# Kernel optimization log

Measured on AMD Instinct MI355X. Metric: run time of the kernel, lower is better.

## Reference

```python
import jax, jax.numpy as jnp
import numpy as np

E = 2048
H = 16
DH = E // H  # 128
B, T = 2, 2048
EPS = 1e-8


def rmsnorm(x, g):
    rms = jnp.sqrt(jnp.mean(x * x, axis=-1, keepdims=True) + EPS)
    return g * (x / rms)


def setup_inputs() -> dict:
    key = jax.random.key(0)
    ks = jax.random.split(key, 16)
    s_in = 1.0 / np.sqrt(E)
    s_ff = 1.0 / np.sqrt(4 * E)
    return {
        "x": jax.random.normal(ks[0], (B, T, E), dtype=jnp.float32),
        # stacked per-head QKV projections, stored (in, out) so y = x @ W + b
        "wq": jax.random.normal(ks[1], (H, E, DH), dtype=jnp.float32) * s_in,
        "bq": jax.random.normal(ks[2], (H, DH), dtype=jnp.float32) * s_in,
        "wk": jax.random.normal(ks[3], (H, E, DH), dtype=jnp.float32) * s_in,
        "bk": jax.random.normal(ks[4], (H, DH), dtype=jnp.float32) * s_in,
        "wv": jax.random.normal(ks[5], (H, E, DH), dtype=jnp.float32) * s_in,
        "bv": jax.random.normal(ks[6], (H, DH), dtype=jnp.float32) * s_in,
        "wo": jax.random.normal(ks[7], (E, E), dtype=jnp.float32) * s_in,
        "bo": jax.random.normal(ks[8], (E,), dtype=jnp.float32) * s_in,
        "w1": jax.random.normal(ks[9], (E, 4 * E), dtype=jnp.float32) * s_in,
        "b1": jax.random.normal(ks[10], (4 * E,), dtype=jnp.float32) * s_in,
        "w2": jax.random.normal(ks[11], (4 * E, E), dtype=jnp.float32) * s_ff,
        "b2": jax.random.normal(ks[12], (E,), dtype=jnp.float32) * s_ff,
        "g1": jnp.ones((E,), dtype=jnp.float32),
        "g2": jnp.ones((E,), dtype=jnp.float32),
    }


def reference(x, wq, bq, wk, bk, wv, bv, wo, bo, w1, b1, w2, b2, g1, g2):
    b, t, e = x.shape
    # --- attention sublayer ---
    h = rmsnorm(x, g1)
    q = jnp.einsum("bte,hed->bhtd", h, wq) + bq[None, :, None, :]
    k = jnp.einsum("bte,hed->bhtd", h, wk) + bk[None, :, None, :]
    v = jnp.einsum("bte,hed->bhtd", h, wv) + bv[None, :, None, :]
    scores = jnp.einsum("bhtd,bhsd->bhts", q, k) / jnp.sqrt(jnp.float32(DH))
    causal = jnp.tril(jnp.ones((t, t), dtype=bool))
    scores = jnp.where(causal[None, None], scores, -jnp.inf)
    w = jax.nn.softmax(scores, axis=-1)
    o = jnp.einsum("bhts,bhsd->bhtd", w, v)
    o = o.transpose(0, 2, 1, 3).reshape(b, t, e)  # concat heads on last dim
    x = x + o @ wo + bo
    # --- FFN sublayer (exact GELU, dropout is identity at inference) ---
    h = rmsnorm(x, g2)
    x = x + jax.nn.gelu(h @ w1 + b1, approximate=False) @ w2 + b2
    return x
```

## Files before the change

kernel.cpp:

```cpp
#include <hip/hip_runtime.h>
#include <hip/hip_bf16.h>

typedef unsigned short u16;
typedef unsigned int   u32;
typedef __attribute__((ext_vector_type(8))) short short8;
typedef __attribute__((ext_vector_type(4))) float f32x4;
typedef __attribute__((ext_vector_type(4))) unsigned short u16x4;

#define E_    2048
#define H_    16
#define DH_   128
#define B_    2
#define T_    2048
#define NTOK  4096
#define QKVN  6144

#define VMCNT(n) asm volatile("s_waitcnt vmcnt(" #n ")" ::: "memory")
#define LGKM0()  asm volatile("s_waitcnt lgkmcnt(0)" ::: "memory")

__device__ __forceinline__ u16 f2bf(float f) {
  union { float f; u32 u; } v; v.f = f;
  u32 r = (v.u + 0x7FFFu + ((v.u >> 16) & 1u)) >> 16;
  return (u16)r;
}

__global__ __launch_bounds__(256) void tr64(
    const float* __restrict__ in, u16* __restrict__ out,
    int R, int C, size_t inZ, size_t outZ)
{
  __shared__ float t[64][65];
  const float* ib = in + (size_t)blockIdx.z * inZ;
  u16* ob = out + (size_t)blockIdx.z * outZ;
  const int r0 = blockIdx.y * 64, c0 = blockIdx.x * 64;
  const int tid = threadIdx.x;
  const int rr = tid >> 4;
  const int cc = (tid & 15) * 4;
  #pragma unroll
  for (int p = 0; p < 4; ++p) {
    const float4 v = *(const float4*)(ib + (size_t)(r0 + p * 16 + rr) * C + c0 + cc);
    t[cc + 0][p * 16 + rr] = v.x;
    t[cc + 1][p * 16 + rr] = v.y;
    t[cc + 2][p * 16 + rr] = v.z;
    t[cc + 3][p * 16 + rr] = v.w;
  }
  __syncthreads();
  const int wr = tid >> 3;
  const int wc = (tid & 7) * 8;
  #pragma unroll
  for (int p = 0; p < 2; ++p) {
    short8 s;
    #pragma unroll
    for (int j = 0; j < 8; ++j) s[j] = (short)f2bf(t[p * 32 + wr][wc + j]);
    *(short8*)(ob + (size_t)(c0 + p * 32 + wr) * R + r0 + wc) = s;
  }
}

__global__ __launch_bounds__(256) void bias_cat(
    const float* __restrict__ bq, const float* __restrict__ bk,
    const float* __restrict__ bv, float* __restrict__ bias)
{
  int idx = blockIdx.x * 256 + threadIdx.x;
  const float* bb = (idx < 2048) ? bq : (idx < 4096) ? bk : bv;
  bias[idx] = bb[idx & 2047];
}

__global__ __launch_bounds__(256) void rmsnorm_k(
    const float* __restrict__ x, const float* __restrict__ g, u16* __restrict__ o)
{
  const int row = blockIdx.x;
  const float4* xr = (const float4*)(x + (size_t)row * E_);
  const float4* gr = (const float4*)g;
  const int tid = threadIdx.x;
  float4 a0 = xr[tid], a1 = xr[tid + 256];
  float s = a0.x*a0.x + a0.y*a0.y + a0.z*a0.z + a0.w*a0.w
          + a1.x*a1.x + a1.y*a1.y + a1.z*a1.z + a1.w*a1.w;
  #pragma unroll
  for (int m = 1; m < 64; m <<= 1) s += __shfl_xor(s, m);
  __shared__ float wsum[4];
  if ((tid & 63) == 0) wsum[tid >> 6] = s;
  __syncthreads();
  float tot = wsum[0] + wsum[1] + wsum[2] + wsum[3];
  float rinv = rsqrtf(tot * (1.0f / E_) + 1e-8f);
  float4 g0 = gr[tid], g1 = gr[tid + 256];
  u16x4 o0, o1;
  o0[0] = f2bf(a0.x * g0.x * rinv); o0[1] = f2bf(a0.y * g0.y * rinv);
  o0[2] = f2bf(a0.z * g0.z * rinv); o0[3] = f2bf(a0.w * g0.w * rinv);
  o1[0] = f2bf(a1.x * g1.x * rinv); o1[1] = f2bf(a1.y * g1.y * rinv);
  o1[2] = f2bf(a1.z * g1.z * rinv); o1[3] = f2bf(a1.w * g1.w * rinv);
  u16x4* orow = (u16x4*)(o + (size_t)row * E_);
  orow[tid] = o0;
  orow[tid + 256] = o1;
}

__device__ __forceinline__ void gload_lds16(const void* g, u16* lds_base) {
  __builtin_amdgcn_global_load_lds(
      (const __attribute__((address_space(1))) u32*)g,
      (__attribute__((address_space(3))) u32*)lds_base, 16, 0, 0);
}

template<int BM, int BN, int EPI>
__global__ __launch_bounds__(512, 2)
void gemm3(const u16* __restrict__ A, const u16* __restrict__ Bt,
           const float* __restrict__ bias, const float* __restrict__ resid,
           void* __restrict__ out, int M, int N, int K)
{
  constexpr int WROWS = BM / 2;
  constexpr int WCOLS = BN / 4;
  constexpr int MR    = WROWS / 16;
  constexpr int BUF   = (BM + BN) * 32;
  __shared__ __align__(16) u16 sh[3 * BUF];

  const int tid  = threadIdx.x;
  const int lane = tid & 63;
  const int l15  = lane & 15, lg = lane >> 4;
  const int w    = tid >> 6;
  const int wm   = w >> 2;
  const int wn   = w & 3;

  const int nbx = N / BN;
  const int nwg = nbx * (M / BM);
  const int q8  = nwg >> 3;
  const int sid = (blockIdx.x & 7) * q8 + (blockIdx.x >> 3);
  const int m0  = (sid / nbx) * BM;
  const int n0  = (sid % nbx) * BN;

  const int r0 = tid >> 2, c0 = (tid & 3) * 8;
  const u16* gA  = A  + (size_t)(m0 + r0) * K + c0;
  const u16* gB  = Bt + (size_t)(n0 + r0) * K + c0;
  const u16* gA2 = gA + (size_t)128 * K;
  const u16* gB2 = gB + (size_t)128 * K;
  const int wub = (tid & ~63) * 8;

  f32x4 acc[MR][4] = {};
  const int NT = K >> 5;

  #pragma unroll
  for (int t = 0; t < 2; ++t) {
    u16* wb = sh + t * BUF;
    const int kS = t * 32;
    if constexpr (BM == 256) {
      gload_lds16(gA  + kS, wb + wub);
      gload_lds16(gA2 + kS, wb + 512 * 8 + wub);
      gload_lds16(gB  + kS, wb + 1024 * 8 + wub);
      gload_lds16(gB2 + kS, wb + 1536 * 8 + wub);
    } else {
      gload_lds16(gA  + kS, wb + wub);
      gload_lds16(gB  + kS, wb + 512 * 8 + wub);
      gload_lds16(gB2 + kS, wb + 1024 * 8 + wub);
    }
  }
  if constexpr (BM == 256) VMCNT(4); else VMCNT(3);
  __builtin_amdgcn_s_barrier();
  __builtin_amdgcn_sched_barrier(0);

  int b0 = 0, b2 = 2;
  #pragma unroll 1
  for (int i = 0; i < NT; ++i) {
    const u16* rb = sh + b0 * BUF;
    u16* wb = sh + b2 * BUF;
    const bool st = (i + 2 < NT);
    const int kS = (i + 2) << 5;
    short8 af[4], bf[4];

    if constexpr (BM == 256) {
      #pragma unroll
      for (int n = 0; n < 4; ++n)
        bf[n] = *(const short8*)(rb + BM * 32 + (wn * WCOLS + n * 16 + l15) * 32 + lg * 8);
      #pragma unroll
      for (int m = 0; m < 4; ++m)
        af[m] = *(const short8*)(rb + (wm * WROWS + m * 16 + l15) * 32 + lg * 8);
      if (st) {
        gload_lds16(gA + kS, wb + wub);
        gload_lds16(gB + kS, wb + 1024 * 8 + wub);
      }
      __builtin_amdgcn_s_barrier();
      LGKM0();
      __builtin_amdgcn_sched_barrier(0);
      __builtin_amdgcn_s_setprio(1);
      #pragma unroll
      for (int m = 0; m < 4; ++m)
        #pragma unroll
        for (int n = 0; n < 4; ++n)
          acc[m][n] = __builtin_amdgcn_mfma_f32_16x16x32_bf16(af[m], bf[n], acc[m][n], 0, 0, 0);
      __builtin_amdgcn_s_setprio(0);
      __builtin_amdgcn_s_barrier();
      __builtin_amdgcn_sched_barrier(0);
      #pragma unroll
      for (int m = 0; m < 4; ++m)
        af[m] = *(const short8*)(rb + (wm * WROWS + (4 + m) * 16 + l15) * 32 + lg * 8);
      if (st) {
        gload_lds16(gA2 + kS, wb + 512 * 8 + wub);
        gload_lds16(gB2 + kS, wb + 1536 * 8 + wub);
      }
      __builtin_amdgcn_s_barrier();
      LGKM0();
      __builtin_amdgcn_sched_barrier(0);
      __builtin_amdgcn_s_setprio(1);
      #pragma unroll
      for (int m = 0; m < 4; ++m)
        #pragma unroll
        for (int n = 0; n < 4; ++n)
          acc[4 + m][n] = __builtin_amdgcn_mfma_f32_16x16x32_bf16(af[m], bf[n], acc[4 + m][n], 0, 0, 0);
      __builtin_amdgcn_s_setprio(0);
      VMCNT(4);
      __builtin_amdgcn_s_barrier();
      __builtin_amdgcn_sched_barrier(0);
    } else {
      #pragma unroll
      for (int n = 0; n < 4; ++n)
        bf[n] = *(const short8*)(rb + BM * 32 + (wn * WCOLS + n * 16 + l15) * 32 + lg * 8);
      #pragma unroll
      for (int m = 0; m < 4; ++m)
        af[m] = *(const short8*)(rb + (wm * WROWS + m * 16 + l15) * 32 + lg * 8);
      if (st) {
        gload_lds16(gA  + kS, wb + wub);
        gload_lds16(gB  + kS, wb + 512 * 8 + wub);
        gload_lds16(gB2 + kS, wb + 1024 * 8 + wub);
      }
      __builtin_amdgcn_s_barrier();
      LGKM0();
      __builtin_amdgcn_sched_barrier(0);
      __builtin_amdgcn_s_setprio(1);
      #pragma unroll
      for (int m = 0; m < 4; ++m)
        #pragma unroll
        for (int n = 0; n < 4; ++n)
          acc[m][n] = __builtin_amdgcn_mfma_f32_16x16x32_bf16(af[m], bf[n], acc[m][n], 0, 0, 0);
      __builtin_amdgcn_s_setprio(0);
      VMCNT(3);
      __builtin_amdgcn_s_barrier();
      __builtin_amdgcn_sched_barrier(0);
    }
    b0 = (b0 == 2) ? 0 : b0 + 1;
    b2 = (b2 == 2) ? 0 : b2 + 1;
  }

  #pragma unroll
  for (int n = 0; n < 4; ++n) {
    const int col = n0 + wn * WCOLS + n * 16 + l15;
    const float bv = bias[col];
    #pragma unroll
    for (int m = 0; m < MR; ++m) {
      #pragma unroll
      for (int r = 0; r < 4; ++r) {
        const int row = m0 + wm * WROWS + m * 16 + lg * 4 + r;
        const size_t off = (size_t)row * N + col;
        float v = acc[m][n][r] + bv;
        if (EPI == 1) {
          ((float*)out)[off] = v + resid[off];
        } else if (EPI == 2) {
          float gg = 0.5f * v * (1.0f + erff(v * 0.70710678118654752f));
          ((u16*)out)[off] = f2bf(gg);
        } else {
          ((u16*)out)[off] = f2bf(v);
        }
      }
    }
  }
}

__global__ __launch_bounds__(256) void vtrans_k(
    const u16* __restrict__ qkv, u16* __restrict__ vt)
{
  __shared__ u16 tile[DH_][66];
  const int tid = threadIdx.x;
  const int bid = blockIdx.x;
  const int tt = bid & 31;
  const int bh = bid >> 5;
  const int b  = bh >> 4, h = bh & 15;
  const int t0 = tt * 64;
  const u16* src = qkv + (size_t)b * T_ * QKVN + 2 * E_ + h * DH_;
  #pragma unroll
  for (int it = 0; it < 8; ++it) {
    int c = it * 256 + tid;
    int t = c >> 5, dc = c & 31;
    u16x4 v = *(const u16x4*)(src + (size_t)(t0 + t) * QKVN + dc * 4);
    #pragma unroll
    for (int j = 0; j < 4; ++j) tile[dc * 4 + j][t] = v[j];
  }
  __syncthreads();
  u16* dst = vt + (size_t)bh * DH_ * T_ + t0;
  #pragma unroll
  for (int it = 0; it < 8; ++it) {
    int c = it * 256 + tid;
    int d = c >> 4, tc = c & 15;
    u16x4 v;
    #pragma unroll
    for (int j = 0; j < 4; ++j) v[j] = tile[d][tc * 4 + j];
    *(u16x4*)(dst + (size_t)d * T_ + tc * 4) = v;
  }
}

__global__ __launch_bounds__(256) void attn_k(
    const u16* __restrict__ qkv, const u16* __restrict__ vt, u16* __restrict__ o)
{
  const int tid  = threadIdx.x;
  const int lane = tid & 63;
  const int w    = tid >> 6;
  const int l15  = lane & 15, lg = lane >> 4;
  const int bid  = blockIdx.x;
  const int pair = bid & 31;
  const int qt   = 15 - (bid >> 5);
  const int h    = pair & 15;
  const int b    = pair >> 4;
  const int Q0 = qt * 128;
  const int qw = Q0 + w * 32;

  __shared__ __align__(16) u16 Ks[2][64 * 128];
  __shared__ __align__(16) u16 Vs[2][128 * 64];
  __shared__ __align__(16) u16 Ps[4][32 * 64];

  const u16* qb  = qkv + (size_t)b * T_ * QKVN + h * DH_;
  const u16* kb  = qb + E_;
  const u16* vtb = vt + (size_t)(b * H_ + h) * DH_ * T_;

  short8 qf[2][4];
  #pragma unroll
  for (int qi = 0; qi < 2; ++qi)
    #pragma unroll
    for (int kk = 0; kk < 4; ++kk)
      qf[qi][kk] = *(const short8*)(qb + (size_t)(qw + qi * 16 + l15) * QKVN + kk * 32 + lg * 8);

  f32x4 oacc[2][8] = {};
  float m_[2][4], l_[2][4];
  #pragma unroll
  for (int qi = 0; qi < 2; ++qi)
    #pragma unroll
    for (int r = 0; r < 4; ++r) { m_[qi][r] = -1e30f; l_[qi][r] = 0.f; }

  const int xr = l15 & 7;
  const float scl = 0.08838834764831845f;
  const int nt = Q0 / 64 + 2;
  const int qmaxw = qw + 31;
  const int wub = (tid & ~63);

  const u16* kp[4]; const u16* vp[4];
  #pragma unroll
  for (int i = 0; i < 4; ++i) {
    int f = i * 256 + tid;
    int r = f >> 4, p = f & 15, c = p ^ (r & 7);
    kp[i] = kb + (size_t)r * QKVN + c * 8;
  }
  #pragma unroll
  for (int i = 0; i < 4; ++i) {
    int f = i * 256 + tid;
    int d = f >> 3, p = f & 7, c = p ^ (d & 7);
    vp[i] = vtb + (size_t)d * T_ + c * 8;
  }

  auto STAGEKV = [&](int s0, int bufi) {
    const size_t ko = (size_t)s0 * QKVN;
    #pragma unroll
    for (int i = 0; i < 4; ++i)
      gload_lds16(kp[i] + ko, &Ks[bufi][(i * 256 + wub) * 8]);
    #pragma unroll
    for (int i = 0; i < 4; ++i)
      gload_lds16(vp[i] + s0, &Vs[bufi][(i * 256 + wub) * 8]);
  };

  STAGEKV(0, 0);
  VMCNT(0);
  __builtin_amdgcn_s_barrier();
  __builtin_amdgcn_sched_barrier(0);

  #pragma unroll 1
  for (int st = 0; st < nt; ++st) {
    const int s0 = st * 64;
    const int cur = st & 1;
    if (st + 1 < nt) STAGEKV(s0 + 64, cur ^ 1);

    if (s0 <= qmaxw) {
      const u16* Kc = Ks[cur];
      const u16* Vc = Vs[cur];
      f32x4 sc[2][4] = {};
      __builtin_amdgcn_s_setprio(1);
      #pragma unroll
      for (int sj = 0; sj < 4; ++sj) {
        const int row = sj * 16 + l15;
        #pragma unroll
        for (int kk = 0; kk < 4; ++kk) {
          short8 kfr = *(const short8*)(Kc + row * 128 + (((kk * 4 + lg) ^ xr) * 8));
          sc[0][sj] = __builtin_amdgcn_mfma_f32_16x16x32_bf16(qf[0][kk], kfr, sc[0][sj], 0, 0, 0);
          sc[1][sj] = __builtin_amdgcn_mfma_f32_16x16x32_bf16(qf[1][kk], kfr, sc[1][sj], 0, 0, 0);
        }
      }
      __builtin_amdgcn_s_setprio(0);
      const bool needmask = (s0 + 63 > qw);
      #pragma unroll
      for (int qi = 0; qi < 2; ++qi)
        #pragma unroll
        for (int sj = 0; sj < 4; ++sj)
          #pragma unroll
          for (int r = 0; r < 4; ++r) {
            float v = sc[qi][sj][r] * scl;
            if (needmask) {
              int s = s0 + sj * 16 + l15;
              int q = qw + qi * 16 + lg * 4 + r;
              if (s > q) v = -1e30f;
            }
            sc[qi][sj][r] = v;
          }
      #pragma unroll
      for (int qi = 0; qi < 2; ++qi) {
        float tmax[4], alpha[4], rsum[4];
        #pragma unroll
        for (int r = 0; r < 4; ++r)
          tmax[r] = fmaxf(fmaxf(sc[qi][0][r], sc[qi][1][r]), fmaxf(sc[qi][2][r], sc[qi][3][r]));
        #pragma unroll
        for (int r = 0; r < 4; ++r)
          #pragma unroll
          for (int m = 1; m < 16; m <<= 1) tmax[r] = fmaxf(tmax[r], __shfl_xor(tmax[r], m));
        #pragma unroll
        for (int r = 0; r < 4; ++r) {
          float mn = fmaxf(m_[qi][r], tmax[r]);
          alpha[r] = __expf(m_[qi][r] - mn);
          m_[qi][r] = mn;
          rsum[r] = 0.f;
        }
        #pragma unroll
        for (int sj = 0; sj < 4; ++sj)
          #pragma unroll
          for (int r = 0; r < 4; ++r) {
            float p = __expf(sc[qi][sj][r] - m_[qi][r]);
            rsum[r] += p;
            const int row = qi * 16 + lg * 4 + r;
            const int ch  = (sj * 2 + (l15 >> 3)) ^ (row & 7);
            Ps[w][row * 64 + ch * 8 + (l15 & 7)] = f2bf(p);
          }
        #pragma unroll
        for (int r = 0; r < 4; ++r) {
          #pragma unroll
          for (int m = 1; m < 16; m <<= 1) rsum[r] += __shfl_xor(rsum[r], m);
          l_[qi][r] = l_[qi][r] * alpha[r] + rsum[r];
        }
        #pragma unroll
        for (int dj = 0; dj < 8; ++dj)
          #pragma unroll
          for (int r = 0; r < 4; ++r) oacc[qi][dj][r] *= alpha[r];
      }
      LGKM0();
      __builtin_amdgcn_sched_barrier(0);
      __builtin_amdgcn_s_setprio(1);
      #pragma unroll
      for (int ks = 0; ks < 2; ++ks) {
        short8 pf0 = *(const short8*)(&Ps[w][l15 * 64 + (((ks * 4 + lg) ^ xr) * 8)]);
        short8 pf1 = *(const short8*)(&Ps[w][(16 + l15) * 64 + (((ks * 4 + lg) ^ xr) * 8)]);
        #pragma unroll
        for (int dj = 0; dj < 8; ++dj) {
          const int row = dj * 16 + l15;
          short8 vfr = *(const short8*)(Vc + row * 64 + (((ks * 4 + lg) ^ xr) * 8));
          oacc[0][dj] = __builtin_amdgcn_mfma_f32_16x16x32_bf16(pf0, vfr, oacc[0][dj], 0, 0, 0);
          oacc[1][dj] = __builtin_amdgcn_mfma_f32_16x16x32_bf16(pf1, vfr, oacc[1][dj], 0, 0, 0);
        }
      }
      __builtin_amdgcn_s_setprio(0);
    }
    VMCNT(0);
    __builtin_amdgcn_s_barrier();
    __builtin_amdgcn_sched_barrier(0);
  }

  float inv[2][4];
  #pragma unroll
  for (int qi = 0; qi < 2; ++qi)
    #pragma unroll
    for (int r = 0; r < 4; ++r) inv[qi][r] = 1.0f / l_[qi][r];
  u16* ob = o + (size_t)(b * T_ + qw) * E_ + h * DH_;
  #pragma unroll
  for (int qi = 0; qi < 2; ++qi)
    #pragma unroll
    for (int dj = 0; dj < 8; ++dj)
      #pragma unroll
      for (int r = 0; r < 4; ++r)
        ob[(size_t)(qi * 16 + lg * 4 + r) * E_ + dj * 16 + l15] = f2bf(oacc[qi][dj][r] * inv[qi][r]);
}

extern "C" void kernel_launch(void* const* d_in, const int* in_sizes, int n_in,
                              void* d_out, int out_size, void* d_ws, size_t ws_size,
                              hipStream_t stream)
{
  const float* x  = (const float*)d_in[0];
  const float* wq = (const float*)d_in[1];
  const float* bq = (const float*)d_in[2];
  const float* wk = (const float*)d_in[3];
  const float* bk = (const float*)d_in[4];
  const float* wv = (const float*)d_in[5];
  const float* bv = (const float*)d_in[6];
  const float* wo = (const float*)d_in[7];
  const float* bo = (const float*)d_in[8];
  const float* w1 = (const float*)d_in[9];
  const float* b1 = (const float*)d_in[10];
  const float* w2 = (const float*)d_in[11];
  const float* b2 = (const float*)d_in[12];
  const float* g1 = (const float*)d_in[13];
  const float* g2 = (const float*)d_in[14];
  float* xout = (float*)d_out;

  if (ws_size < 201351168u) return;

  char* ws = (char*)d_ws;
  u16*   wqkv_t = (u16*)(ws + 0);
  u16*   h1     = (u16*)(ws + 25165824);
  u16*   qkv    = (u16*)(ws + 41943040);
  u16*   vt     = (u16*)(ws + 92274688);
  u16*   o_     = (u16*)(ws + 109051904);
  u16*   wo_t   = (u16*)(ws + 125829120);
  u16*   w1_t   = (u16*)(ws + 134217728);
  u16*   w2_t   = (u16*)(ws + 167772160);
  float* bqkv   = (float*)(ws + 201326592);
  u16*   u_     = (u16*)(ws + 0);
  u16*   h2     = vt;
  float* x2     = xout;

  tr64<<<dim3(2, 32, 16), 256, 0, stream>>>(wq, wqkv_t,                          E_, DH_, (size_t)E_ * DH_, (size_t)DH_ * E_);
  tr64<<<dim3(2, 32, 16), 256, 0, stream>>>(wk, wqkv_t + (size_t)E_ * E_,        E_, DH_, (size_t)E_ * DH_, (size_t)DH_ * E_);
  tr64<<<dim3(2, 32, 16), 256, 0, stream>>>(wv, wqkv_t + (size_t)2 * E_ * E_,    E_, DH_, (size_t)E_ * DH_, (size_t)DH_ * E_);
  tr64<<<dim3(32, 32, 1),  256, 0, stream>>>(wo, wo_t, E_, E_, 0, 0);
  tr64<<<dim3(128, 32, 1), 256, 0, stream>>>(w1, w1_t, E_, 4 * E_, 0, 0);
  tr64<<<dim3(32, 128, 1), 256, 0, stream>>>(w2, w2_t, 4 * E_, E_, 0, 0);
  bias_cat<<<24, 256, 0, stream>>>(bq, bk, bv, bqkv);

  rmsnorm_k<<<NTOK, 256, 0, stream>>>(x, g1, h1);
  gemm3<256, 256, 0><<<(NTOK / 256) * (QKVN / 256), 512, 0, stream>>>(h1, wqkv_t, bqkv, nullptr, qkv, NTOK, QKVN, E_);
  vtrans_k<<<B_ * H_ * (T_ / 64), 256, 0, stream>>>(qkv, vt);
  attn_k<<<B_ * H_ * (T_ / 16 / 8), 256, 0, stream>>>(qkv, vt, o_);
  gemm3<128, 256, 1><<<(NTOK / 128) * (E_ / 256), 512, 0, stream>>>(o_, wo_t, bo, x, x2, NTOK, E_, E_);
  rmsnorm_k<<<NTOK, 256, 0, stream>>>(x2, g2, h2);
  gemm3<256, 256, 2><<<(NTOK / 256) * (4 * E_ / 256), 512, 0, stream>>>(h2, w1_t, b1, nullptr, u_, NTOK, 4 * E_, E_);
  gemm3<128, 256, 1><<<(NTOK / 128) * (E_ / 256), 512, 0, stream>>>(u_, w2_t, b2, x2, xout, NTOK, E_, 4 * E_);
}
```

Before: 762.0 us.

## Swizzle GEMM LDS layout, stage bf16 epilogue through LDS, shrink QKV tile

After: 728.3 us. 1.05x faster.

```diff
diff --git a/kernel.cpp b/kernel.cpp
--- a/kernel.cpp
+++ b/kernel.cpp
@@ -116,6 +116,7 @@
   const int w    = tid >> 6;
   const int wm   = w >> 2;
   const int wn   = w & 3;
+  const int xs   = (l15 >> 1) & 3;
 
   const int nbx = N / BN;
   const int nwg = nbx * (M / BM);
@@ -124,7 +125,8 @@
   const int m0  = (sid / nbx) * BM;
   const int n0  = (sid % nbx) * BN;
 
-  const int r0 = tid >> 2, c0 = (tid & 3) * 8;
+  const int r0 = tid >> 2;
+  const int c0 = (((tid & 3) ^ ((tid >> 3) & 3)) * 8);
   const u16* gA  = A  + (size_t)(m0 + r0) * K + c0;
   const u16* gB  = Bt + (size_t)(n0 + r0) * K + c0;
   const u16* gA2 = gA + (size_t)128 * K;
@@ -165,10 +167,10 @@
     if constexpr (BM == 256) {
       #pragma unroll
       for (int n = 0; n < 4; ++n)
-        bf[n] = *(const short8*)(rb + BM * 32 + (wn * WCOLS + n * 16 + l15) * 32 + lg * 8);
+        bf[n] = *(const short8*)(rb + BM * 32 + (wn * WCOLS + n * 16 + l15) * 32 + ((lg ^ xs) * 8));
       #pragma unroll
       for (int m = 0; m < 4; ++m)
-        af[m] = *(const short8*)(rb + (wm * WROWS + m * 16 + l15) * 32 + lg * 8);
+        af[m] = *(const short8*)(rb + (wm * WROWS + m * 16 + l15) * 32 + ((lg ^ xs) * 8));
       if (st) {
         gload_lds16(gA + kS, wb + wub);
         gload_lds16(gB + kS, wb + 1024 * 8 + wub);
@@ -187,7 +189,7 @@
       __builtin_amdgcn_sched_barrier(0);
       #pragma unroll
       for (int m = 0; m < 4; ++m)
-        af[m] = *(const short8*)(rb + (wm * WROWS + (4 + m) * 16 + l15) * 32 + lg * 8);
+        af[m] = *(const short8*)(rb + (wm * WROWS + (4 + m) * 16 + l15) * 32 + ((lg ^ xs) * 8));
       if (st) {
         gload_lds16(gA2 + kS, wb + 512 * 8 + wub);
         gload_lds16(gB2 + kS, wb + 1536 * 8 + wub);
@@ -208,10 +210,10 @@
     } else {
       #pragma unroll
       for (int n = 0; n < 4; ++n)
-        bf[n] = *(const short8*)(rb + BM * 32 + (wn * WCOLS + n * 16 + l15) * 32 + lg * 8);
+        bf[n] = *(const short8*)(rb + BM * 32 + (wn * WCOLS + n * 16 + l15) * 32 + ((lg ^ xs) * 8));
       #pragma unroll
       for (int m = 0; m < 4; ++m)
-        af[m] = *(const short8*)(rb + (wm * WROWS + m * 16 + l15) * 32 + lg * 8);
+        af[m] = *(const short8*)(rb + (wm * WROWS + m * 16 + l15) * 32 + ((lg ^ xs) * 8));
       if (st) {
         gload_lds16(gA  + kS, wb + wub);
         gload_lds16(gB  + kS, wb + 512 * 8 + wub);
@@ -235,25 +237,46 @@
     b2 = (b2 == 2) ? 0 : b2 + 1;
   }
 
-  #pragma unroll
-  for (int n = 0; n < 4; ++n) {
-    const int col = n0 + wn * WCOLS + n * 16 + l15;
-    const float bv = bias[col];
+  float bv[4];
+  #pragma unroll
+  for (int n = 0; n < 4; ++n) bv[n] = bias[n0 + wn * WCOLS + n * 16 + l15];
+
+  if constexpr (EPI == 1) {
+    #pragma unroll
+    for (int n = 0; n < 4; ++n) {
+      const int col = n0 + wn * WCOLS + n * 16 + l15;
+      #pragma unroll
+      for (int m = 0; m < MR; ++m)
+        #pragma unroll
+        for (int r = 0; r < 4; ++r) {
+          const int row = m0 + wm * WROWS + m * 16 + lg * 4 + r;
+          const size_t off = (size_t)row * N + col;
+          ((float*)out)[off] = acc[m][n][r] + bv[n] + resid[off];
+        }
+    }
+  } else {
+    u16* ep = sh + w * 1024;
     #pragma unroll
     for (int m = 0; m < MR; ++m) {
-      #pragma unroll
-      for (int r = 0; r < 4; ++r) {
-        const int row = m0 + wm * WROWS + m * 16 + lg * 4 + r;
-        const size_t off = (size_t)row * N + col;
-        float v = acc[m][n][r] + bv;
-        if (EPI == 1) {
-          ((float*)out)[off] = v + resid[off];
-        } else if (EPI == 2) {
-          float gg = 0.5f * v * (1.0f + erff(v * 0.70710678118654752f));
-          ((u16*)out)[off] = f2bf(gg);
-        } else {
-          ((u16*)out)[off] = f2bf(v);
+      LGKM0();
+      __builtin_amdgcn_sched_barrier(0);
+      #pragma unroll
+      for (int n = 0; n < 4; ++n)
+        #pragma unroll
+        for (int r = 0; r < 4; ++r) {
+          float v = acc[m][n][r] + bv[n];
+          if (EPI == 2) v = 0.5f * v * (1.0f + erff(v * 0.70710678118654752f));
+          ep[(lg * 4 + r) * 64 + n * 16 + l15] = f2bf(v);
         }
+      LGKM0();
+      __builtin_amdgcn_sched_barrier(0);
+      const int row0 = m0 + wm * WROWS + m * 16;
+      #pragma unroll
+      for (int it = 0; it < 2; ++it) {
+        const int ch = it * 64 + lane;
+        const int rr = ch >> 3, c8 = ch & 7;
+        short8 s = *(const short8*)(ep + rr * 64 + c8 * 8);
+        *(short8*)((u16*)out + (size_t)(row0 + rr) * N + n0 + wn * WCOLS + c8 * 8) = s;
       }
     }
   }
@@ -521,7 +544,7 @@
   bias_cat<<<24, 256, 0, stream>>>(bq, bk, bv, bqkv);
 
   rmsnorm_k<<<NTOK, 256, 0, stream>>>(x, g1, h1);
-  gemm3<256, 256, 0><<<(NTOK / 256) * (QKVN / 256), 512, 0, stream>>>(h1, wqkv_t, bqkv, nullptr, qkv, NTOK, QKVN, E_);
+  gemm3<128, 256, 0><<<(NTOK / 128) * (QKVN / 256), 512, 0, stream>>>(h1, wqkv_t, bqkv, nullptr, qkv, NTOK, QKVN, E_);
   vtrans_k<<<B_ * H_ * (T_ / 64), 256, 0, stream>>>(qkv, vt);
   attn_k<<<B_ * H_ * (T_ / 16 / 8), 256, 0, stream>>>(qkv, vt, o_);
   gemm3<128, 256, 1><<<(NTOK / 128) * (E_ / 256), 512, 0, stream>>>(o_, wo_t, bo, x, x2, NTOK, E_, E_);
```
